# Kernel tuning notes

Hardware: AMD Instinct MI355X
Metric: run time of the kernel (lower is better)

The kernel has to match this reference:

```python
import jax, jax.numpy as jnp
import numpy as np

N, E = 50000, 800000
HID, EDIM, HEADS = 256, 64, 8
C = HID // HEADS  # per-head channels = 32
NEG_SLOPE = 0.2
LN_EPS = 1e-5


def setup_inputs() -> dict:
    key = jax.random.key(0)
    ks = jax.random.split(key, 12)
    s = 1.0 / np.sqrt(HID)
    se = 1.0 / np.sqrt(EDIM)
    return {
        "x": jax.random.normal(ks[0], (N, HID), jnp.float32),
        "edge_index": jax.random.randint(ks[1], (2, E), 0, N, jnp.int32),
        "edge_attr": jax.random.normal(ks[2], (E, EDIM), jnp.float32),
        "W": jax.random.uniform(ks[3], (HID, HEADS * C), jnp.float32, -s, s),
        "W_e": jax.random.uniform(ks[4], (EDIM, HEADS * C), jnp.float32, -se, se),
        "att_src": jax.random.normal(ks[5], (HEADS, C), jnp.float32) * 0.1,
        "att_dst": jax.random.normal(ks[6], (HEADS, C), jnp.float32) * 0.1,
        "att_edge": jax.random.normal(ks[7], (HEADS, C), jnp.float32) * 0.1,
        "bias": jnp.zeros((HEADS * C,), jnp.float32),
        "gamma": jnp.ones((HID,), jnp.float32),
        "beta": jnp.zeros((HID,), jnp.float32),
    }


def _gat_block(x, edge_index, edge_attr, W, W_e, att_src, att_dst, att_edge, bias, gamma, beta):
    n = x.shape[0]
    src, dst = edge_index[0], edge_index[1]
    # node projection (shared for src/dst, as in PyG GATConv non-bipartite)
    xp = (x @ W).reshape(n, HEADS, C)                       # [N,H,C]
    a_src = jnp.einsum("nhc,hc->nh", xp, att_src)          # [N,H]
    a_dst = jnp.einsum("nhc,hc->nh", xp, att_dst)          # [N,H]
    ep = (edge_attr @ W_e).reshape(-1, HEADS, C)            # [E,H,C]
    a_edge = jnp.einsum("ehc,hc->eh", ep, att_edge)        # [E,H]
    # per-edge attention logit + LeakyReLU
    alpha = a_src[src] + a_dst[dst] + a_edge                # [E,H]
    alpha = jax.nn.leaky_relu(alpha, NEG_SLOPE)
    # segment softmax over incoming edges of each dst node
    m = jax.ops.segment_max(alpha, dst, num_segments=n)     # [N,H]
    m = jnp.where(jnp.isfinite(m), m, 0.0)
    ea = jnp.exp(alpha - m[dst])
    den = jax.ops.segment_sum(ea, dst, num_segments=n)      # [N,H]
    attn = ea / (den[dst] + 1e-16)                          # [E,H]
    # weighted message + scatter-add
    msg = xp[src] * attn[:, :, None]                        # [E,H,C]
    out = jax.ops.segment_sum(msg, dst, num_segments=n)     # [N,H,C]
    h = out.reshape(n, HEADS * C) + bias
    # residual + LayerNorm (dropout in eval mode -> identity)
    y = x + h
    mu = jnp.mean(y, axis=-1, keepdims=True)
    var = jnp.var(y, axis=-1, keepdims=True)
    return (y - mu) * jax.lax.rsqrt(var + LN_EPS) * gamma + beta


def reference(x, edge_index, edge_attr, W, W_e, att_src, att_dst, att_edge, bias, gamma, beta):
    return _gat_block(x, edge_index, edge_attr, W, W_e, att_src, att_dst, att_edge, bias, gamma, beta)
```

## Files before the change

kernel.cpp:

```cpp
#include <hip/hip_runtime.h>
#include <cstdint>

#define NEG_SLOPE 0.2f
#define LN_EPS 1e-5f

typedef __bf16 bf16x8 __attribute__((ext_vector_type(8)));
typedef float f32x4 __attribute__((ext_vector_type(4)));

__device__ __forceinline__ float b2f(unsigned int u) {
    union { unsigned int i; float f; } x; x.i = u << 16; return x.f;
}
__device__ __forceinline__ unsigned short f2b(float f) {
    union { float f; unsigned int i; } x; x.f = f;
    unsigned int r = x.i + 0x7fffu + ((x.i >> 16) & 1u);
    return (unsigned short)(r >> 16);
}

__global__ void k0a_prep(const float* __restrict__ W,
                         const float* __restrict__ We,
                         const float* __restrict__ att_src,
                         const float* __restrict__ att_dst,
                         const float* __restrict__ att_edge,
                         float* __restrict__ u_src, float* __restrict__ u_dst,
                         float* __restrict__ vW) {
    int t = threadIdx.x;
    const float* wr = W + t * 256;
    for (int h = 0; h < 8; h++) {
        float s1 = 0.f, s2 = 0.f;
        for (int c = 0; c < 32; c++) {
            float w = wr[h * 32 + c];
            s1 += w * att_src[h * 32 + c];
            s2 += w * att_dst[h * 32 + c];
        }
        u_src[t * 8 + h] = s1; u_dst[t * 8 + h] = s2;
    }
    if (t < 64) {
        const float* er = We + t * 256;
        for (int h = 0; h < 8; h++) {
            float s = 0.f;
            for (int c = 0; c < 32; c++) s += er[h * 32 + c] * att_edge[h * 32 + c];
            vW[t * 8 + h] = s;
        }
    }
}

__global__ void k0b_wfrag(const float* __restrict__ W,
                          unsigned short* __restrict__ Wf) {
    int T = blockIdx.x * 256 + threadIdx.x;
    int j    = T & 7;
    int lane = (T >> 3) & 63;
    int kk   = (T >> 9) & 7;
    int i    = (T >> 12) & 3;
    int w    = T >> 14;
    int n = w * 64 + i * 16 + (lane & 15);
    int k = kk * 32 + (lane >> 4) * 8 + j;
    Wf[T] = f2b(W[k * 256 + n]);
}

__global__ __launch_bounds__(256) void k1_xp(const float* __restrict__ x,
                                             const unsigned short* __restrict__ Wf,
                                             const float* __restrict__ u_src,
                                             const float* __restrict__ u_dst,
                                             unsigned short* __restrict__ xp,
                                             float* __restrict__ a_src,
                                             float* __restrict__ a_dst, int N) {
    __shared__ float red[2][4][16][8];
    int m0 = blockIdx.x * 16;
    int lane = threadIdx.x & 63, wave = threadIdx.x >> 6;
    int quad = lane >> 4, l16 = lane & 15;
    int mrow = m0 + l16; if (mrow > N - 1) mrow = N - 1;
    const float* ap = x + (size_t)mrow * 256 + quad * 8;
    const unsigned short* wfw = Wf + (size_t)wave * 16384;
    f32x4 ac0 = {0,0,0,0}, ac1 = {0,0,0,0}, ac2 = {0,0,0,0}, ac3 = {0,0,0,0};
    float pas[8] = {0,0,0,0,0,0,0,0}, pad_[8] = {0,0,0,0,0,0,0,0};
#pragma unroll
    for (int kk = 0; kk < 8; kk++) {
        float4 fa0 = *(const float4*)(ap + kk * 32);
        float4 fa1 = *(const float4*)(ap + kk * 32 + 4);
        if ((kk >> 1) == wave) {
            float f[8] = {fa0.x, fa0.y, fa0.z, fa0.w, fa1.x, fa1.y, fa1.z, fa1.w};
#pragma unroll
            for (int j = 0; j < 8; j++) {
                int k = kk * 32 + quad * 8 + j;
                const float4* up = (const float4*)(u_src + k * 8);
                float4 s0 = up[0], s1 = up[1];
                const float4* vp = (const float4*)(u_dst + k * 8);
                float4 d0 = vp[0], d1 = vp[1];
                pas[0] += f[j] * s0.x; pas[1] += f[j] * s0.y;
                pas[2] += f[j] * s0.z; pas[3] += f[j] * s0.w;
                pas[4] += f[j] * s1.x; pas[5] += f[j] * s1.y;
                pas[6] += f[j] * s1.z; pas[7] += f[j] * s1.w;
                pad_[0] += f[j] * d0.x; pad_[1] += f[j] * d0.y;
                pad_[2] += f[j] * d0.z; pad_[3] += f[j] * d0.w;
                pad_[4] += f[j] * d1.x; pad_[5] += f[j] * d1.y;
                pad_[6] += f[j] * d1.z; pad_[7] += f[j] * d1.w;
            }
        }
        union { unsigned short u[8]; bf16x8 v; } A;
        A.u[0] = f2b(fa0.x); A.u[1] = f2b(fa0.y); A.u[2] = f2b(fa0.z); A.u[3] = f2b(fa0.w);
        A.u[4] = f2b(fa1.x); A.u[5] = f2b(fa1.y); A.u[6] = f2b(fa1.z); A.u[7] = f2b(fa1.w);
        const unsigned short* wk = wfw + kk * 512 + lane * 8;
        bf16x8 b0 = *(const bf16x8*)(wk);
        bf16x8 b1 = *(const bf16x8*)(wk + 4096);
        bf16x8 b2 = *(const bf16x8*)(wk + 8192);
        bf16x8 b3 = *(const bf16x8*)(wk + 12288);
        ac0 = __builtin_amdgcn_mfma_f32_16x16x32_bf16(A.v, b0, ac0, 0, 0, 0);
        ac1 = __builtin_amdgcn_mfma_f32_16x16x32_bf16(A.v, b1, ac1, 0, 0, 0);
        ac2 = __builtin_amdgcn_mfma_f32_16x16x32_bf16(A.v, b2, ac2, 0, 0, 0);
        ac3 = __builtin_amdgcn_mfma_f32_16x16x32_bf16(A.v, b3, ac3, 0, 0, 0);
    }
#pragma unroll
    for (int h = 0; h < 8; h++) {
        pas[h] += __shfl_xor(pas[h], 16, 64);
        pas[h] += __shfl_xor(pas[h], 32, 64);
        pad_[h] += __shfl_xor(pad_[h], 16, 64);
        pad_[h] += __shfl_xor(pad_[h], 32, 64);
    }
    if (quad == 0) {
#pragma unroll
        for (int h = 0; h < 8; h++) {
            red[0][wave][l16][h] = pas[h];
            red[1][wave][l16][h] = pad_[h];
        }
    }
    int nb = wave * 64;
#pragma unroll
    for (int r = 0; r < 4; r++) {
        int m = m0 + quad * 4 + r;
        if (m < N) {
            unsigned short* op = xp + (size_t)m * 256 + nb + l16;
            op[0]  = f2b(ac0[r]); op[16] = f2b(ac1[r]);
            op[32] = f2b(ac2[r]); op[48] = f2b(ac3[r]);
        }
    }
    __syncthreads();
    {
        int t = threadIdx.x;
        int arr = t >> 7, r = (t >> 3) & 15, h = t & 7;
        int m = m0 + r;
        if (m < N) {
            float sum = red[arr][0][r][h] + red[arr][1][r][h]
                      + red[arr][2][r][h] + red[arr][3][r][h];
            (arr ? a_dst : a_src)[m * 8 + h] = sum;
        }
    }
}

__global__ __launch_bounds__(256) void k2_edge(const int* __restrict__ ei,
                                               const float* __restrict__ eattr,
                                               const float* __restrict__ vW,
                                               const float* __restrict__ a_src,
                                               const float* __restrict__ a_dst,
                                               unsigned short* __restrict__ ea,
                                               int* __restrict__ deg, int E) {
    __shared__ float sv[2048];
    int t = threadIdx.x;
    if (t < 128) {
        const float4* g = (const float4*)vW;
        float4* s4 = (float4*)sv;
        int k = t >> 1, half = t & 1;
        int kl = ((k & 15) << 2) | (k >> 4);
        s4[kl * 2 + half] = g[t];
    }
    __syncthreads();
    int e = blockIdx.x * 64 + (t >> 2), kp = t & 3;
    if (e >= E) return;
    const float4* ar = (const float4*)(eattr + (size_t)e * 64 + kp * 16);
    float acc[8] = {0,0,0,0,0,0,0,0};
#pragma unroll
    for (int q = 0; q < 4; q++) {
        float4 u = ar[q];
        float f[4] = {u.x, u.y, u.z, u.w};
#pragma unroll
        for (int j = 0; j < 4; j++) {
            int kl = ((q * 4 + j) << 2) | kp;
            const float4* vp = (const float4*)(sv + kl * 8);
            float4 v0 = vp[0], v1 = vp[1];
            acc[0] += f[j] * v0.x; acc[1] += f[j] * v0.y;
            acc[2] += f[j] * v0.z; acc[3] += f[j] * v0.w;
            acc[4] += f[j] * v1.x; acc[5] += f[j] * v1.y;
            acc[6] += f[j] * v1.z; acc[7] += f[j] * v1.w;
        }
    }
#pragma unroll
    for (int h = 0; h < 8; h++) {
        acc[h] += __shfl_xor(acc[h], 1, 64);
        acc[h] += __shfl_xor(acc[h], 2, 64);
    }
    int s = ei[e], d = ei[E + e];
    float2 asv = *(const float2*)(a_src + s * 8 + kp * 2);
    float2 adv = *(const float2*)(a_dst + d * 8 + kp * 2);
    float l0 = asv.x + adv.x + acc[kp * 2];
    float l1 = asv.y + adv.y + acc[kp * 2 + 1];
    l0 = (l0 > 0.f) ? l0 : NEG_SLOPE * l0;
    l1 = (l1 > 0.f) ? l1 : NEG_SLOPE * l1;
    unsigned int pk = (unsigned)f2b(__expf(l0)) | ((unsigned)f2b(__expf(l1)) << 16);
    ((unsigned int*)ea)[(size_t)e * 4 + kp] = pk;
    if (kp == 0) atomicAdd(deg + d, 1);
}

__global__ __launch_bounds__(1024) void k3a_scan(const int* __restrict__ deg,
                                                 int* __restrict__ rowptr,
                                                 int* __restrict__ bsum, int N) {
    __shared__ int s[1024];
    int t = threadIdx.x, i = blockIdx.x * 1024 + t;
    int v = (i < N) ? deg[i] : 0;
    s[t] = v; __syncthreads();
    for (int off = 1; off < 1024; off <<= 1) {
        int add = (t >= off) ? s[t - off] : 0;
        __syncthreads();
        s[t] += add;
        __syncthreads();
    }
    if (i < N) rowptr[i] = s[t] - v;
    if (t == 1023) bsum[blockIdx.x] = s[1023];
}
__global__ void k3b_scan(const int* __restrict__ bsum, int* __restrict__ boff, int nb) {
    if (threadIdx.x == 0) {
        int run = 0;
        for (int i = 0; i < nb; i++) { boff[i] = run; run += bsum[i]; }
    }
}
__global__ __launch_bounds__(1024) void k3c_add(int* __restrict__ rowptr,
                                                int* __restrict__ cursor,
                                                const int* __restrict__ boff, int N, int E) {
    int i = blockIdx.x * 1024 + threadIdx.x;
    if (i < N) {
        int r = rowptr[i] + boff[blockIdx.x];
        rowptr[i] = r; cursor[i] = r;
    }
    if (i == 0) rowptr[N] = E;
}
__global__ __launch_bounds__(256) void k3d_scatter(const int* __restrict__ ei,
                                                   int* __restrict__ cursor,
                                                   int* __restrict__ perm, int E) {
    int e = blockIdx.x * 256 + threadIdx.x;
    if (e >= E) return;
    int d = ei[E + e];
    int p = atomicAdd(cursor + d, 1);
    perm[p] = e;
}

__global__ __launch_bounds__(64) void k4_agg(const float* __restrict__ xin,
                                             const unsigned short* __restrict__ xp,
                                             const unsigned short* __restrict__ ea,
                                             const int* __restrict__ rowptr,
                                             const int* __restrict__ perm,
                                             const int* __restrict__ ei,
                                             const float* __restrict__ bias,
                                             const float* __restrict__ gamma,
                                             const float* __restrict__ beta,
                                             float* __restrict__ out, int N) {
    __shared__ int ssrc[64];
    __shared__ float sattn[64 * 9];
    int n = blockIdx.x, l = threadIdx.x;
    int start = rowptr[n], end = rowptr[n + 1];

    float dl[8] = {0,0,0,0,0,0,0,0};
    for (int base = start; base < end; base += 64) {
        if (base + l < end) {
            int e = perm[base + l];
            uint4 u = ((const uint4*)ea)[e];
            dl[0] += b2f(u.x & 0xffffu); dl[1] += b2f(u.x >> 16);
            dl[2] += b2f(u.y & 0xffffu); dl[3] += b2f(u.y >> 16);
            dl[4] += b2f(u.z & 0xffffu); dl[5] += b2f(u.z >> 16);
            dl[6] += b2f(u.w & 0xffffu); dl[7] += b2f(u.w >> 16);
        }
    }
#pragma unroll
    for (int off = 32; off > 0; off >>= 1) {
#pragma unroll
        for (int j = 0; j < 8; j++) dl[j] += __shfl_xor(dl[j], off, 64);
    }
    float sinv[8];
#pragma unroll
    for (int j = 0; j < 8; j++) sinv[j] = 1.0f / (dl[j] + 1e-16f);

    float a0 = 0.f, a1 = 0.f, a2 = 0.f, a3 = 0.f;
    int hh = l >> 3;
    for (int base = start; base < end; base += 64) {
        int cnt = end - base; if (cnt > 64) cnt = 64;
        if (l < cnt) {
            int e = perm[base + l];
            ssrc[l] = ei[e];
            uint4 u = ((const uint4*)ea)[e];
            float* sp = sattn + l * 9;
            sp[0] = b2f(u.x & 0xffffu) * sinv[0]; sp[1] = b2f(u.x >> 16) * sinv[1];
            sp[2] = b2f(u.y & 0xffffu) * sinv[2]; sp[3] = b2f(u.y >> 16) * sinv[3];
            sp[4] = b2f(u.z & 0xffffu) * sinv[4]; sp[5] = b2f(u.z >> 16) * sinv[5];
            sp[6] = b2f(u.w & 0xffffu) * sinv[6]; sp[7] = b2f(u.w >> 16) * sinv[7];
        }
        __syncthreads();
        for (int i = 0; i < cnt; i++) {
            int s = ssrc[i];
            uint2 u = *(const uint2*)(xp + (size_t)s * 256 + l * 4);
            float w = sattn[i * 9 + hh];
            a0 += b2f(u.x & 0xffffu) * w; a1 += b2f(u.x >> 16) * w;
            a2 += b2f(u.y & 0xffffu) * w; a3 += b2f(u.y >> 16) * w;
        }
        __syncthreads();
    }
    float4 xv = *(const float4*)(xin + (size_t)n * 256 + l * 4);
    float4 bv = *(const float4*)(bias + l * 4);
    float y0 = xv.x + a0 + bv.x;
    float y1 = xv.y + a1 + bv.y;
    float y2 = xv.z + a2 + bv.z;
    float y3 = xv.w + a3 + bv.w;
    float s1 = y0 + y1 + y2 + y3;
    float s2 = y0 * y0 + y1 * y1 + y2 * y2 + y3 * y3;
#pragma unroll
    for (int o = 32; o > 0; o >>= 1) {
        s1 += __shfl_down(s1, o, 64);
        s2 += __shfl_down(s2, o, 64);
    }
    s1 = __shfl(s1, 0, 64); s2 = __shfl(s2, 0, 64);
    float mu = s1 * (1.f / 256.f);
    float var = s2 * (1.f / 256.f) - mu * mu;
    float rs = rsqrtf(var + LN_EPS);
    float4 gv  = *(const float4*)(gamma + l * 4);
    float4 btv = *(const float4*)(beta + l * 4);
    float4 ov;
    ov.x = (y0 - mu) * rs * gv.x + btv.x;
    ov.y = (y1 - mu) * rs * gv.y + btv.y;
    ov.z = (y2 - mu) * rs * gv.z + btv.z;
    ov.w = (y3 - mu) * rs * gv.w + btv.w;
    *(float4*)(out + (size_t)n * 256 + l * 4) = ov;
}

extern "C" void kernel_launch(void* const* d_in, const int* in_sizes, int n_in,
                              void* d_out, int out_size, void* d_ws, size_t ws_size,
                              hipStream_t stream) {
    const float* x     = (const float*)d_in[0];
    const int*   ei    = (const int*)d_in[1];
    const float* eattr = (const float*)d_in[2];
    const float* W     = (const float*)d_in[3];
    const float* We    = (const float*)d_in[4];
    const float* atts  = (const float*)d_in[5];
    const float* attd  = (const float*)d_in[6];
    const float* atte  = (const float*)d_in[7];
    const float* bias  = (const float*)d_in[8];
    const float* gamma = (const float*)d_in[9];
    const float* beta  = (const float*)d_in[10];
    float* out = (float*)d_out;
    int N = in_sizes[0] / 256;
    int E = in_sizes[1] / 2;

    char* p = (char*)d_ws;
    auto carve = [&](size_t bytes) -> void* {
        void* r = (void*)p; p += (bytes + 255) & ~(size_t)255; return r;
    };
    unsigned short* xp = (unsigned short*)carve((size_t)N * 256 * 2);
    unsigned short* ea = (unsigned short*)carve((size_t)E * 8 * 2);
    float* a_src       = (float*)carve((size_t)N * 8 * 4);
    float* a_dst       = (float*)carve((size_t)N * 8 * 4);
    int*   deg         = (int*)carve((size_t)N * 4);
    int*   rowptr      = (int*)carve((size_t)(N + 1) * 4);
    int*   cursor      = (int*)carve((size_t)N * 4);
    int*   perm        = (int*)carve((size_t)E * 4);
    int*   bsum        = (int*)carve(1024);
    int*   boff        = (int*)carve(1024);
    float* u_src       = (float*)carve(2048 * 4);
    float* u_dst       = (float*)carve(2048 * 4);
    float* vW          = (float*)carve(512 * 4);
    unsigned short* Wf = (unsigned short*)carve(65536 * 2);

    hipMemsetAsync(deg, 0, (size_t)N * 4, stream);

    hipLaunchKernelGGL(k0a_prep, dim3(1), dim3(256), 0, stream,
                       W, We, atts, attd, atte, u_src, u_dst, vW);
    hipLaunchKernelGGL(k0b_wfrag, dim3(256), dim3(256), 0, stream, W, Wf);
    hipLaunchKernelGGL(k1_xp, dim3((N + 15) / 16), dim3(256), 0, stream,
                       x, Wf, u_src, u_dst, xp, a_src, a_dst, N);
    hipLaunchKernelGGL(k2_edge, dim3((E + 63) / 64), dim3(256), 0, stream,
                       ei, eattr, vW, a_src, a_dst, ea, deg, E);
    int nb = (N + 1023) / 1024;
    hipLaunchKernelGGL(k3a_scan, dim3(nb), dim3(1024), 0, stream, deg, rowptr, bsum, N);
    hipLaunchKernelGGL(k3b_scan, dim3(1), dim3(64), 0, stream, bsum, boff, nb);
    hipLaunchKernelGGL(k3c_add, dim3(nb), dim3(1024), 0, stream, rowptr, cursor, boff, N, E);
    hipLaunchKernelGGL(k3d_scatter, dim3((E + 255) / 256), dim3(256), 0, stream,
                       ei, cursor, perm, E);
    hipLaunchKernelGGL(k4_agg, dim3(N), dim3(64), 0, stream,
                       x, xp, ea, rowptr, perm, ei, bias, gamma, beta, out, N);
}
```

Before: 610.8 us.

## Split per-node aggregation across four waves and fold softmax normalisation

The aggregation kernel now runs 256 threads per destination node. The four waves split that node's incoming edges and combine their partial sums through shared memory. The separate pass that summed the softmax denominator is removed: the denominator is accumulated while edge weights are staged, and normalisation is applied once to the final sum. The block-offset scan also changes from a single-thread serial loop to a wave shuffle scan. The aim is more memory-level parallelism per node and fewer reads of the edge-attention array, at the cost of extra shared-memory reduction, idle waves for low-degree nodes, and a scan that assumes at most 64 blocks.

```diff
diff --git a/kernel.cpp b/kernel.cpp
--- a/kernel.cpp
+++ b/kernel.cpp
@@ -216,10 +216,15 @@
     if (t == 1023) bsum[blockIdx.x] = s[1023];
 }
 __global__ void k3b_scan(const int* __restrict__ bsum, int* __restrict__ boff, int nb) {
-    if (threadIdx.x == 0) {
-        int run = 0;
-        for (int i = 0; i < nb; i++) { boff[i] = run; run += bsum[i]; }
-    }
+    int l = threadIdx.x;
+    int v = (l < nb) ? bsum[l] : 0;
+    int x = v;
+#pragma unroll
+    for (int off = 1; off < 64; off <<= 1) {
+        int y = __shfl_up(x, off, 64);
+        if (l >= off) x += y;
+    }
+    if (l < nb) boff[l] = x - v;
 }
 __global__ __launch_bounds__(1024) void k3c_add(int* __restrict__ rowptr,
                                                 int* __restrict__ cursor,
@@ -241,71 +246,76 @@
     perm[p] = e;
 }
 
-__global__ __launch_bounds__(64) void k4_agg(const float* __restrict__ xin,
-                                             const unsigned short* __restrict__ xp,
-                                             const unsigned short* __restrict__ ea,
-                                             const int* __restrict__ rowptr,
-                                             const int* __restrict__ perm,
-                                             const int* __restrict__ ei,
-                                             const float* __restrict__ bias,
-                                             const float* __restrict__ gamma,
-                                             const float* __restrict__ beta,
-                                             float* __restrict__ out, int N) {
+__global__ __launch_bounds__(256) void k4_agg(const float* __restrict__ xin,
+                                              const unsigned short* __restrict__ xp,
+                                              const unsigned short* __restrict__ ea,
+                                              const int* __restrict__ rowptr,
+                                              const int* __restrict__ perm,
+                                              const int* __restrict__ ei,
+                                              const float* __restrict__ bias,
+                                              const float* __restrict__ gamma,
+                                              const float* __restrict__ beta,
+                                              float* __restrict__ out, int N) {
     __shared__ int ssrc[64];
-    __shared__ float sattn[64 * 9];
-    int n = blockIdx.x, l = threadIdx.x;
+    __shared__ float sea[64 * 9];
+    __shared__ float racc[4][64][4];
+    __shared__ float rden[8];
+    int n = blockIdx.x;
+    int t = threadIdx.x, wave = t >> 6, l = t & 63;
     int start = rowptr[n], end = rowptr[n + 1];
-
-    float dl[8] = {0,0,0,0,0,0,0,0};
-    for (int base = start; base < end; base += 64) {
-        if (base + l < end) {
-            int e = perm[base + l];
-            uint4 u = ((const uint4*)ea)[e];
-            dl[0] += b2f(u.x & 0xffffu); dl[1] += b2f(u.x >> 16);
-            dl[2] += b2f(u.y & 0xffffu); dl[3] += b2f(u.y >> 16);
-            dl[4] += b2f(u.z & 0xffffu); dl[5] += b2f(u.z >> 16);
-            dl[6] += b2f(u.w & 0xffffu); dl[7] += b2f(u.w >> 16);
-        }
-    }
-#pragma unroll
-    for (int off = 32; off > 0; off >>= 1) {
-#pragma unroll
-        for (int j = 0; j < 8; j++) dl[j] += __shfl_xor(dl[j], off, 64);
-    }
-    float sinv[8];
-#pragma unroll
-    for (int j = 0; j < 8; j++) sinv[j] = 1.0f / (dl[j] + 1e-16f);
-
+    int hh = l >> 3;
     float a0 = 0.f, a1 = 0.f, a2 = 0.f, a3 = 0.f;
-    int hh = l >> 3;
+    float den[8] = {0,0,0,0,0,0,0,0};
     for (int base = start; base < end; base += 64) {
         int cnt = end - base; if (cnt > 64) cnt = 64;
-        if (l < cnt) {
-            int e = perm[base + l];
-            ssrc[l] = ei[e];
+        if (t < cnt) {
+            int e = perm[base + t];
+            ssrc[t] = ei[e];
             uint4 u = ((const uint4*)ea)[e];
-            float* sp = sattn + l * 9;
-            sp[0] = b2f(u.x & 0xffffu) * sinv[0]; sp[1] = b2f(u.x >> 16) * sinv[1];
-            sp[2] = b2f(u.y & 0xffffu) * sinv[2]; sp[3] = b2f(u.y >> 16) * sinv[3];
-            sp[4] = b2f(u.z & 0xffffu) * sinv[4]; sp[5] = b2f(u.z >> 16) * sinv[5];
-            sp[6] = b2f(u.w & 0xffffu) * sinv[6]; sp[7] = b2f(u.w >> 16) * sinv[7];
+            float v0 = b2f(u.x & 0xffffu), v1 = b2f(u.x >> 16);
+            float v2 = b2f(u.y & 0xffffu), v3 = b2f(u.y >> 16);
+            float v4 = b2f(u.z & 0xffffu), v5 = b2f(u.z >> 16);
+            float v6 = b2f(u.w & 0xffffu), v7 = b2f(u.w >> 16);
+            float* sp = sea + t * 9;
+            sp[0] = v0; sp[1] = v1; sp[2] = v2; sp[3] = v3;
+            sp[4] = v4; sp[5] = v5; sp[6] = v6; sp[7] = v7;
+            den[0] += v0; den[1] += v1; den[2] += v2; den[3] += v3;
+            den[4] += v4; den[5] += v5; den[6] += v6; den[7] += v7;
         }
         __syncthreads();
-        for (int i = 0; i < cnt; i++) {
+        for (int i = wave; i < cnt; i += 4) {
             int s = ssrc[i];
             uint2 u = *(const uint2*)(xp + (size_t)s * 256 + l * 4);
-            float w = sattn[i * 9 + hh];
+            float w = sea[i * 9 + hh];
             a0 += b2f(u.x & 0xffffu) * w; a1 += b2f(u.x >> 16) * w;
             a2 += b2f(u.y & 0xffffu) * w; a3 += b2f(u.y >> 16) * w;
         }
         __syncthreads();
     }
+    racc[wave][l][0] = a0; racc[wave][l][1] = a1;
+    racc[wave][l][2] = a2; racc[wave][l][3] = a3;
+    if (wave == 0) {
+#pragma unroll
+        for (int off = 32; off > 0; off >>= 1) {
+#pragma unroll
+            for (int j = 0; j < 8; j++) den[j] += __shfl_xor(den[j], off, 64);
+        }
+        if (l < 8) rden[l] = den[l];
+    }
+    __syncthreads();
+    if (wave != 0) return;
+    float m0 = racc[0][l][0] + racc[1][l][0] + racc[2][l][0] + racc[3][l][0];
+    float m1 = racc[0][l][1] + racc[1][l][1] + racc[2][l][1] + racc[3][l][1];
+    float m2 = racc[0][l][2] + racc[1][l][2] + racc[2][l][2] + racc[3][l][2];
+    float m3 = racc[0][l][3] + racc[1][l][3] + racc[2][l][3] + racc[3][l][3];
+    float sinv = 1.0f / (rden[hh] + 1e-16f);
+    m0 *= sinv; m1 *= sinv; m2 *= sinv; m3 *= sinv;
     float4 xv = *(const float4*)(xin + (size_t)n * 256 + l * 4);
     float4 bv = *(const float4*)(bias + l * 4);
-    float y0 = xv.x + a0 + bv.x;
-    float y1 = xv.y + a1 + bv.y;
-    float y2 = xv.z + a2 + bv.z;
-    float y3 = xv.w + a3 + bv.w;
+    float y0 = xv.x + m0 + bv.x;
+    float y1 = xv.y + m1 + bv.y;
+    float y2 = xv.z + m2 + bv.z;
+    float y3 = xv.w + m3 + bv.w;
     float s1 = y0 + y1 + y2 + y3;
     float s2 = y0 * y0 + y1 * y1 + y2 * y2 + y3 * y3;
 #pragma unroll
@@ -379,6 +389,6 @@
     hipLaunchKernelGGL(k3c_add, dim3(nb), dim3(1024), 0, stream, rowptr, cursor, boff, N, E);
     hipLaunchKernelGGL(k3d_scatter, dim3((E + 255) / 256), dim3(256), 0, stream,
                        ei, cursor, perm, E);
-    hipLaunchKernelGGL(k4_agg, dim3(N), dim3(64), 0, stream,
+    hipLaunchKernelGGL(k4_agg, dim3(N), dim3(256), 0, stream,
                        x, xp, ea, rowptr, perm, ei, bias, gamma, beta, out, N);
 }
```

After: 622.5 us. Within noise of the previous version (+1.9%).
